# Kernel optimization log

Hardware: AMD Instinct MI355X
Metric: run time of the kernel (lower is better)

Reference implementation:

```python
import jax, jax.numpy as jnp
import numpy as np

H = 64  # hidden size
T, B, I = 512, 4096, 2


def gru_layer(x_seq, Wih, Whh, bih, bhh):
    """PyTorch-semantics GRU layer. x_seq: [T,B,in]. Returns (all_h [T,B,H], h_last [B,H])."""
    # Precompute input-side gates for all timesteps in one GEMM: [T,B,3H]
    xg = jnp.einsum('tbi,gi->tbg', x_seq, Wih) + bih
    h0 = jnp.zeros((x_seq.shape[1], H), dtype=x_seq.dtype)

    def step(h, xg_t):
        hg = h @ Whh.T + bhh  # [B,3H]
        r = jax.nn.sigmoid(xg_t[:, :H] + hg[:, :H])
        z = jax.nn.sigmoid(xg_t[:, H:2 * H] + hg[:, H:2 * H])
        n = jnp.tanh(xg_t[:, 2 * H:] + r * hg[:, 2 * H:])
        h_new = (1.0 - z) * n + z * h
        return h_new, h_new

    h_last, hs = jax.lax.scan(step, h0, xg)
    return hs, h_last


def setup_inputs() -> dict:
    key = jax.random.key(0)
    ks = jax.random.split(key, 12)
    s = 0.125  # ~1/sqrt(H), matches PyTorch uniform init scale
    inp = {
        'x': jax.random.normal(ks[0], (T, B, I), dtype=jnp.float32),
        'Wih0': jax.random.normal(ks[1], (3 * H, I), dtype=jnp.float32) * s,
        'Whh0': jax.random.normal(ks[2], (3 * H, H), dtype=jnp.float32) * s,
        'bih0': jax.random.normal(ks[3], (3 * H,), dtype=jnp.float32) * s,
        'bhh0': jax.random.normal(ks[4], (3 * H,), dtype=jnp.float32) * s,
        'Wih1': jax.random.normal(ks[5], (3 * H, H), dtype=jnp.float32) * s,
        'Whh1': jax.random.normal(ks[6], (3 * H, H), dtype=jnp.float32) * s,
        'bih1': jax.random.normal(ks[7], (3 * H,), dtype=jnp.float32) * s,
        'bhh1': jax.random.normal(ks[8], (3 * H,), dtype=jnp.float32) * s,
        'Wp': jax.random.normal(ks[9], (1, 2 * H), dtype=jnp.float32) * s,
        'bp': jax.random.normal(ks[10], (1,), dtype=jnp.float32) * s,
    }
    return inp


def reference(x, Wih0, Whh0, bih0, bhh0, Wih1, Whh1, bih1, bhh1, Wp, bp):
    hs0, h0f = gru_layer(x, Wih0, Whh0, bih0, bhh0)     # layer 0 over input
    _, h1f = gru_layer(hs0, Wih1, Whh1, bih1, bhh1)      # layer 1 over layer-0 outputs
    feat = jnp.concatenate([h0f, h1f], axis=-1)          # h_n.permute(1,0,2).flatten(1) -> [B, 2H]
    out = feat @ Wp.T + bp                               # [B,1]
    return out.reshape(-1)
```

## Files before the change

### kernel.cpp

```cpp
#include <hip/hip_runtime.h>
#include <stdint.h>

#define TSTEPS 512
#define BATCH  4096

typedef __attribute__((ext_vector_type(8))) short bf16x8;
typedef __attribute__((ext_vector_type(4))) float f32x4;
typedef __attribute__((ext_vector_type(2))) float f32x2;

#define SRZ (-1.4426950408889634f)
#define SN  ( 2.8853900817779268f)
#define SROW 76

__device__ __forceinline__ short f2bf(float f) {
    uint32_t u = __float_as_uint(f);
    uint32_t r = (u + 0x7fffu + ((u >> 16) & 1u)) >> 16;
    return (short)r;
}
__device__ __forceinline__ uint32_t cvt_pk_bf16(float a, float b) {
    uint32_t r;
    asm("v_cvt_pk_bf16_f32 %0, %1, %2" : "=v"(r) : "v"(a), "v"(b));
    return r;
}
__device__ __forceinline__ float fast_rcp(float x) { return __builtin_amdgcn_rcpf(x); }
#if __has_builtin(__builtin_amdgcn_exp2f)
__device__ __forceinline__ float exp2_fast(float x) { return __builtin_amdgcn_exp2f(x); }
#else
__device__ __forceinline__ float exp2_fast(float x) { return __expf(x * 0.6931471805599453f); }
#endif

__device__ __forceinline__ f32x2 fma2(f32x2 a, f32x2 b, f32x2 c) {
    return __builtin_elementwise_fma(a, b, c);
}
__device__ __forceinline__ f32x2 splat2(float s) { return (f32x2){s, s}; }
__device__ __forceinline__ f32x2 exp22(f32x2 y) {
    return (f32x2){exp2_fast(y[0]), exp2_fast(y[1])};
}
__device__ __forceinline__ f32x2 rcp2(f32x2 y) {
    return (f32x2){fast_rcp(y[0]), fast_rcp(y[1])};
}
__device__ __forceinline__ f32x2 sig2(f32x2 y) {
    return rcp2(exp22(y) + splat2(1.0f));
}
__device__ __forceinline__ f32x2 gru_h(f32x2 yz, f32x2 yn, f32x2 h) {
    const f32x2 A = exp22(yz);
    const f32x2 B = exp22(yn);
    const f32x2 P = A * B;
    const f32x2 u = (P - A) + fma2(h, B, h);
    const f32x2 d = (P + A) + (B + splat2(1.0f));
    return u * rcp2(d);
}
__device__ __forceinline__ void bar_lgkm() {
    asm volatile("s_waitcnt lgkmcnt(0)\n\ts_barrier" ::: "memory");
}

__global__ __launch_bounds__(512, 2) void gru_fused(
    const float* __restrict__ x,
    const float* __restrict__ Wih0,
    const float* __restrict__ Whh0,
    const float* __restrict__ bih0,
    const float* __restrict__ bhh0,
    const float* __restrict__ Wih1,
    const float* __restrict__ Whh1,
    const float* __restrict__ bih1,
    const float* __restrict__ bhh1,
    const float* __restrict__ Wp,
    const float* __restrict__ bp,
    float* __restrict__ out)
{
    const int tid  = threadIdx.x;
    const int wv   = tid >> 6;
    const int isL0 = (wv < 4);
    const int w4   = wv & 3;
    const int l    = tid & 63;
    const int lm   = l & 15;
    const int lq   = l >> 4;
    const int b0   = blockIdx.x * 16;
    const int j    = w4 * 16 + lm;

    __shared__ short h0A[2][16 * SROW];
    __shared__ short h1A[2][16 * SROW];
    __shared__ float Pf[16][64];

    for (int idx = tid; idx < 2 * 16 * SROW; idx += 512) {
        ((short*)h0A)[idx] = 0;
        ((short*)h1A)[idx] = 0;
    }
    __syncthreads();

    const int aoff = lm * SROW + lq * 8;
    const int r0   = lq * 4;

    if (isL0) {
        bf16x8 w0[3][2];
#pragma unroll
        for (int g = 0; g < 3; ++g) {
            const int row = g * 64 + j;
            const float sc = (g == 2) ? SN : SRZ;
#pragma unroll
            for (int q = 0; q < 2; ++q) {
                const float* p = Whh0 + row * 64 + q * 32 + lq * 8;
                bf16x8 vh;
#pragma unroll
                for (int i = 0; i < 8; ++i) vh[i] = f2bf(p[i] * sc);
                w0[g][q] = vh;
            }
        }
        const f32x2 wr0 = splat2(SRZ * Wih0[j * 2 + 0]), wr1 = splat2(SRZ * Wih0[j * 2 + 1]);
        const f32x2 wz0 = splat2(SRZ * Wih0[(64 + j) * 2 + 0]), wz1 = splat2(SRZ * Wih0[(64 + j) * 2 + 1]);
        const f32x2 wn0 = splat2(SN * Wih0[(128 + j) * 2 + 0]), wn1 = splat2(SN * Wih0[(128 + j) * 2 + 1]);
        const float cb[3] = { SRZ * (bih0[j] + bhh0[j]),
                              SRZ * (bih0[64 + j] + bhh0[64 + j]),
                              SN  * bhh0[128 + j] };
        const f32x2 bn = splat2(SN * bih0[128 + j]);

        f32x2 h01 = {0.f, 0.f}, h23 = {0.f, 0.f};
        const float* xp = x + (size_t)(b0 + r0) * 2;
        f32x4 xa = *(const f32x4*)xp;
        f32x4 xb = *(const f32x4*)(xp + 4);
        f32x4 xan = xa, xbn = xb;

        for (int t = 0; t <= TSTEPS; ++t) {
            const int pr = t & 1, pw = pr ^ 1;
            bf16x8 a00 = *(const bf16x8*)&h0A[pr][aoff];
            bf16x8 a01 = *(const bf16x8*)&h0A[pr][aoff + 32];

            if (t + 1 < TSTEPS) {
                xp += (size_t)BATCH * 2;
                xan = *(const f32x4*)xp;
                xbn = *(const f32x4*)(xp + 4);
            }

            f32x4 hg0[3];
            __builtin_amdgcn_s_setprio(1);
#pragma unroll
            for (int g = 0; g < 3; ++g) {
                const f32x4 ci = {cb[g], cb[g], cb[g], cb[g]};
                f32x4 c;
                c = __builtin_amdgcn_mfma_f32_16x16x32_bf16(a00, w0[g][0], ci, 0, 0, 0);
                hg0[g] = __builtin_amdgcn_mfma_f32_16x16x32_bf16(a01, w0[g][1], c, 0, 0, 0);
            }
            __builtin_amdgcn_s_setprio(0);

            if (t < TSTEPS) {
                {
                    const f32x2 x0v = {xa[0], xa[2]}, x1v = {xa[1], xa[3]};
                    const f32x2 hgr = {hg0[0][0], hg0[0][1]};
                    const f32x2 hgz = {hg0[1][0], hg0[1][1]};
                    const f32x2 hgn = {hg0[2][0], hg0[2][1]};
                    const f32x2 rv = sig2(fma2(wr0, x0v, fma2(wr1, x1v, hgr)));
                    const f32x2 yz = fma2(wz0, x0v, fma2(wz1, x1v, hgz));
                    const f32x2 yn = fma2(rv, hgn, fma2(wn0, x0v, fma2(wn1, x1v, bn)));
                    const f32x2 hv = gru_h(yz, yn, h01);
                    h01 = hv;
                    const uint32_t pk = cvt_pk_bf16(hv[0], hv[1]);
                    h0A[pw][(r0 + 0) * SROW + j] = (short)(pk & 0xffffu);
                    h0A[pw][(r0 + 1) * SROW + j] = (short)(pk >> 16);
                }
                {
                    const f32x2 x0v = {xb[0], xb[2]}, x1v = {xb[1], xb[3]};
                    const f32x2 hgr = {hg0[0][2], hg0[0][3]};
                    const f32x2 hgz = {hg0[1][2], hg0[1][3]};
                    const f32x2 hgn = {hg0[2][2], hg0[2][3]};
                    const f32x2 rv = sig2(fma2(wr0, x0v, fma2(wr1, x1v, hgr)));
                    const f32x2 yz = fma2(wz0, x0v, fma2(wz1, x1v, hgz));
                    const f32x2 yn = fma2(rv, hgn, fma2(wn0, x0v, fma2(wn1, x1v, bn)));
                    const f32x2 hv = gru_h(yz, yn, h23);
                    h23 = hv;
                    const uint32_t pk = cvt_pk_bf16(hv[0], hv[1]);
                    h0A[pw][(r0 + 2) * SROW + j] = (short)(pk & 0xffffu);
                    h0A[pw][(r0 + 3) * SROW + j] = (short)(pk >> 16);
                }
            }
            xa = xan; xb = xbn;
            bar_lgkm();
        }

        const float wp0 = Wp[j];
        Pf[r0 + 0][j] = wp0 * h01[0];
        Pf[r0 + 1][j] = wp0 * h01[1];
        Pf[r0 + 2][j] = wp0 * h23[0];
        Pf[r0 + 3][j] = wp0 * h23[1];
        __syncthreads();
        __syncthreads();
    } else {
        bf16x8 w1[3][2], w2[3][2];
#pragma unroll
        for (int g = 0; g < 3; ++g) {
            const int row = g * 64 + j;
            const float sc = (g == 2) ? SN : SRZ;
#pragma unroll
            for (int q = 0; q < 2; ++q) {
                const float* p1 = Wih1 + row * 64 + q * 32 + lq * 8;
                const float* p2 = Whh1 + row * 64 + q * 32 + lq * 8;
                bf16x8 v1, v2;
#pragma unroll
                for (int i = 0; i < 8; ++i) {
                    v1[i] = f2bf(p1[i] * sc);
                    v2[i] = f2bf(p2[i] * sc);
                }
                w1[g][q] = v1; w2[g][q] = v2;
            }
        }
        const float cb[3] = { SRZ * (bih1[j] + bhh1[j]),
                              SRZ * (bih1[64 + j] + bhh1[64 + j]),
                              SN  * bih1[128 + j] };
        const float ce2 = SN * bhh1[128 + j];

        f32x2 h01 = {0.f, 0.f}, h23 = {0.f, 0.f};

        for (int t = 0; t <= TSTEPS; ++t) {
            const int pr = t & 1, pw = pr ^ 1;
            bf16x8 a10 = *(const bf16x8*)&h1A[pr][aoff];
            bf16x8 a11 = *(const bf16x8*)&h1A[pr][aoff + 32];

            f32x4 xg1[3], hg1[3];
            __builtin_amdgcn_s_setprio(1);
#pragma unroll
            for (int g = 0; g < 3; ++g) {
                const float ev = (g == 2) ? ce2 : 0.0f;
                const f32x4 ei = {ev, ev, ev, ev};
                f32x4 e;
                e = __builtin_amdgcn_mfma_f32_16x16x32_bf16(a10, w2[g][0], ei, 0, 0, 0);
                hg1[g] = __builtin_amdgcn_mfma_f32_16x16x32_bf16(a11, w2[g][1], e, 0, 0, 0);
            }
            __builtin_amdgcn_s_setprio(0);

            bf16x8 a00 = *(const bf16x8*)&h0A[pr][aoff];
            bf16x8 a01 = *(const bf16x8*)&h0A[pr][aoff + 32];

            __builtin_amdgcn_s_setprio(1);
#pragma unroll
            for (int g = 0; g < 3; ++g) {
                const f32x4 ci = {cb[g], cb[g], cb[g], cb[g]};
                f32x4 d;
                d = __builtin_amdgcn_mfma_f32_16x16x32_bf16(a00, w1[g][0], ci, 0, 0, 0);
                xg1[g] = __builtin_amdgcn_mfma_f32_16x16x32_bf16(a01, w1[g][1], d, 0, 0, 0);
            }
            __builtin_amdgcn_s_setprio(0);

            if (t > 0) {
                {
                    const f32x2 xgr = {xg1[0][0], xg1[0][1]}, hgr = {hg1[0][0], hg1[0][1]};
                    const f32x2 xgz = {xg1[1][0], xg1[1][1]}, hgz = {hg1[1][0], hg1[1][1]};
                    const f32x2 xgn = {xg1[2][0], xg1[2][1]}, hgn = {hg1[2][0], hg1[2][1]};
                    const f32x2 rv = sig2(xgr + hgr);
                    const f32x2 yz = xgz + hgz;
                    const f32x2 yn = fma2(rv, hgn, xgn);
                    const f32x2 hv = gru_h(yz, yn, h01);
                    h01 = hv;
                    const uint32_t pk = cvt_pk_bf16(hv[0], hv[1]);
                    h1A[pw][(r0 + 0) * SROW + j] = (short)(pk & 0xffffu);
                    h1A[pw][(r0 + 1) * SROW + j] = (short)(pk >> 16);
                }
                {
                    const f32x2 xgr = {xg1[0][2], xg1[0][3]}, hgr = {hg1[0][2], hg1[0][3]};
                    const f32x2 xgz = {xg1[1][2], xg1[1][3]}, hgz = {hg1[1][2], hg1[1][3]};
                    const f32x2 xgn = {xg1[2][2], xg1[2][3]}, hgn = {hg1[2][2], hg1[2][3]};
                    const f32x2 rv = sig2(xgr + hgr);
                    const f32x2 yz = xgz + hgz;
                    const f32x2 yn = fma2(rv, hgn, xgn);
                    const f32x2 hv = gru_h(yz, yn, h23);
                    h23 = hv;
                    const uint32_t pk = cvt_pk_bf16(hv[0], hv[1]);
                    h1A[pw][(r0 + 2) * SROW + j] = (short)(pk & 0xffffu);
                    h1A[pw][(r0 + 3) * SROW + j] = (short)(pk >> 16);
                }
            }
            bar_lgkm();
        }

        __syncthreads();
        const float wp1 = Wp[64 + j];
        Pf[r0 + 0][j] += wp1 * h01[0];
        Pf[r0 + 1][j] += wp1 * h01[1];
        Pf[r0 + 2][j] += wp1 * h23[0];
        Pf[r0 + 3][j] += wp1 * h23[1];
        __syncthreads();
    }

    if (tid < 16) {
        float s = bp[0];
#pragma unroll 8
        for (int k = 0; k < 64; ++k) s += Pf[tid][k];
        out[b0 + tid] = s;
    }
}

extern "C" void kernel_launch(void* const* d_in, const int* in_sizes, int n_in,
                              void* d_out, int out_size, void* d_ws, size_t ws_size,
                              hipStream_t stream) {
    (void)in_sizes; (void)n_in; (void)out_size; (void)d_ws; (void)ws_size;
    gru_fused<<<dim3(BATCH / 16), dim3(512), 0, stream>>>(
        (const float*)d_in[0], (const float*)d_in[1], (const float*)d_in[2],
        (const float*)d_in[3], (const float*)d_in[4], (const float*)d_in[5],
        (const float*)d_in[6], (const float*)d_in[7], (const float*)d_in[8],
        (const float*)d_in[9], (const float*)d_in[10], (float*)d_out);
}
```

Before: 337.3 us.

## Unroll GRU time loops by two and precompute layer-0 input gates a step ahead

The layer-0 loop is unrolled by two with even/odd register sets, so the input-projection FMAs for step t+1 are computed while step t's MFMA results are pending. This removes that work from the dependent elementwise chain. Layer 1 is also unrolled by two, with all four LDS A-fragment loads hoisted together and a single priority region around its MFMAs. Its extra trailing iteration is peeled to drop the branch and the unneeded final store. Register pressure rises from the doubled x prefetch and precomputed gate state.

```diff
diff --git a/kernel.cpp b/kernel.cpp
--- a/kernel.cpp
+++ b/kernel.cpp
@@ -3,6 +3,7 @@
 
 #define TSTEPS 512
 #define BATCH  4096
+#define SROW 76
 
 typedef __attribute__((ext_vector_type(8))) short bf16x8;
 typedef __attribute__((ext_vector_type(4))) float f32x4;
@@ -10,7 +11,8 @@
 
 #define SRZ (-1.4426950408889634f)
 #define SN  ( 2.8853900817779268f)
-#define SROW 76
+
+struct PX { f32x2 gr0, gz0, gn0, gr1, gz1, gn1; };
 
 __device__ __forceinline__ short f2bf(float f) {
     uint32_t u = __float_as_uint(f);
@@ -115,22 +117,37 @@
         const f32x2 bn = splat2(SN * bih0[128 + j]);
 
         f32x2 h01 = {0.f, 0.f}, h23 = {0.f, 0.f};
-        const float* xp = x + (size_t)(b0 + r0) * 2;
-        f32x4 xa = *(const f32x4*)xp;
-        f32x4 xb = *(const f32x4*)(xp + 4);
-        f32x4 xan = xa, xbn = xb;
-
-        for (int t = 0; t <= TSTEPS; ++t) {
-            const int pr = t & 1, pw = pr ^ 1;
-            bf16x8 a00 = *(const bf16x8*)&h0A[pr][aoff];
-            bf16x8 a01 = *(const bf16x8*)&h0A[pr][aoff + 32];
-
-            if (t + 1 < TSTEPS) {
+
+        const float* xb_ = x + (size_t)(b0 + r0) * 2;
+        f32x4 xEa = *(const f32x4*)xb_;
+        f32x4 xEb = *(const f32x4*)(xb_ + 4);
+        f32x4 xOa = *(const f32x4*)(xb_ + (size_t)BATCH * 2);
+        f32x4 xOb = *(const f32x4*)(xb_ + (size_t)BATCH * 2 + 4);
+        const float* xp = xb_ + 2 * (size_t)BATCH * 2;
+
+        PX pE, pO;
+        {
+            const f32x2 x0a = {xEa[0], xEa[2]}, x1a = {xEa[1], xEa[3]};
+            const f32x2 x0b = {xEb[0], xEb[2]}, x1b = {xEb[1], xEb[3]};
+            pE.gr0 = fma2(wr0, x0a, wr1 * x1a);
+            pE.gz0 = fma2(wz0, x0a, wz1 * x1a);
+            pE.gn0 = fma2(wn0, x0a, fma2(wn1, x1a, bn));
+            pE.gr1 = fma2(wr0, x0b, wr1 * x1b);
+            pE.gz1 = fma2(wz0, x0b, wz1 * x1b);
+            pE.gn1 = fma2(wn0, x0b, fma2(wn1, x1b, bn));
+        }
+
+        auto l0_step = [&](int pr, bool doload, PX& u, PX& d,
+                           f32x4& xla, f32x4& xlb,
+                           const f32x4& xsa, const f32x4& xsb) {
+            const int pw = pr ^ 1;
+            const bf16x8 a00 = *(const bf16x8*)&h0A[pr][aoff];
+            const bf16x8 a01 = *(const bf16x8*)&h0A[pr][aoff + 32];
+            if (doload) {
+                xla = *(const f32x4*)xp;
+                xlb = *(const f32x4*)(xp + 4);
                 xp += (size_t)BATCH * 2;
-                xan = *(const f32x4*)xp;
-                xbn = *(const f32x4*)(xp + 4);
-            }
-
+            }
             f32x4 hg0[3];
             __builtin_amdgcn_s_setprio(1);
 #pragma unroll
@@ -141,38 +158,45 @@
                 hg0[g] = __builtin_amdgcn_mfma_f32_16x16x32_bf16(a01, w0[g][1], c, 0, 0, 0);
             }
             __builtin_amdgcn_s_setprio(0);
-
-            if (t < TSTEPS) {
-                {
-                    const f32x2 x0v = {xa[0], xa[2]}, x1v = {xa[1], xa[3]};
-                    const f32x2 hgr = {hg0[0][0], hg0[0][1]};
-                    const f32x2 hgz = {hg0[1][0], hg0[1][1]};
-                    const f32x2 hgn = {hg0[2][0], hg0[2][1]};
-                    const f32x2 rv = sig2(fma2(wr0, x0v, fma2(wr1, x1v, hgr)));
-                    const f32x2 yz = fma2(wz0, x0v, fma2(wz1, x1v, hgz));
-                    const f32x2 yn = fma2(rv, hgn, fma2(wn0, x0v, fma2(wn1, x1v, bn)));
-                    const f32x2 hv = gru_h(yz, yn, h01);
-                    h01 = hv;
-                    const uint32_t pk = cvt_pk_bf16(hv[0], hv[1]);
-                    h0A[pw][(r0 + 0) * SROW + j] = (short)(pk & 0xffffu);
-                    h0A[pw][(r0 + 1) * SROW + j] = (short)(pk >> 16);
-                }
-                {
-                    const f32x2 x0v = {xb[0], xb[2]}, x1v = {xb[1], xb[3]};
-                    const f32x2 hgr = {hg0[0][2], hg0[0][3]};
-                    const f32x2 hgz = {hg0[1][2], hg0[1][3]};
-                    const f32x2 hgn = {hg0[2][2], hg0[2][3]};
-                    const f32x2 rv = sig2(fma2(wr0, x0v, fma2(wr1, x1v, hgr)));
-                    const f32x2 yz = fma2(wz0, x0v, fma2(wz1, x1v, hgz));
-                    const f32x2 yn = fma2(rv, hgn, fma2(wn0, x0v, fma2(wn1, x1v, bn)));
-                    const f32x2 hv = gru_h(yz, yn, h23);
-                    h23 = hv;
-                    const uint32_t pk = cvt_pk_bf16(hv[0], hv[1]);
-                    h0A[pw][(r0 + 2) * SROW + j] = (short)(pk & 0xffffu);
-                    h0A[pw][(r0 + 3) * SROW + j] = (short)(pk >> 16);
-                }
-            }
-            xa = xan; xb = xbn;
+            {
+                const f32x2 x0a = {xsa[0], xsa[2]}, x1a = {xsa[1], xsa[3]};
+                const f32x2 x0b = {xsb[0], xsb[2]}, x1b = {xsb[1], xsb[3]};
+                d.gr0 = fma2(wr0, x0a, wr1 * x1a);
+                d.gz0 = fma2(wz0, x0a, wz1 * x1a);
+                d.gn0 = fma2(wn0, x0a, fma2(wn1, x1a, bn));
+                d.gr1 = fma2(wr0, x0b, wr1 * x1b);
+                d.gz1 = fma2(wz0, x0b, wz1 * x1b);
+                d.gn1 = fma2(wn0, x0b, fma2(wn1, x1b, bn));
+            }
+            {
+                const f32x2 hgr = {hg0[0][0], hg0[0][1]};
+                const f32x2 hgz = {hg0[1][0], hg0[1][1]};
+                const f32x2 hgn = {hg0[2][0], hg0[2][1]};
+                const f32x2 rv = sig2(hgr + u.gr0);
+                const f32x2 hv = gru_h(hgz + u.gz0, fma2(rv, hgn, u.gn0), h01);
+                h01 = hv;
+                const uint32_t pk = cvt_pk_bf16(hv[0], hv[1]);
+                h0A[pw][(r0 + 0) * SROW + j] = (short)(pk & 0xffffu);
+                h0A[pw][(r0 + 1) * SROW + j] = (short)(pk >> 16);
+            }
+            {
+                const f32x2 hgr = {hg0[0][2], hg0[0][3]};
+                const f32x2 hgz = {hg0[1][2], hg0[1][3]};
+                const f32x2 hgn = {hg0[2][2], hg0[2][3]};
+                const f32x2 rv = sig2(hgr + u.gr1);
+                const f32x2 hv = gru_h(hgz + u.gz1, fma2(rv, hgn, u.gn1), h23);
+                h23 = hv;
+                const uint32_t pk = cvt_pk_bf16(hv[0], hv[1]);
+                h0A[pw][(r0 + 2) * SROW + j] = (short)(pk & 0xffffu);
+                h0A[pw][(r0 + 3) * SROW + j] = (short)(pk >> 16);
+            }
+        };
+
+        for (int tp = 0; tp < TSTEPS / 2; ++tp) {
+            const bool doload = (tp < TSTEPS / 2 - 1);
+            l0_step(0, doload, pE, pO, xEa, xEb, xOa, xOb);
+            bar_lgkm();
+            l0_step(1, doload, pO, pE, xOa, xOb, xEa, xEb);
             bar_lgkm();
         }
 
@@ -209,10 +233,12 @@
 
         f32x2 h01 = {0.f, 0.f}, h23 = {0.f, 0.f};
 
-        for (int t = 0; t <= TSTEPS; ++t) {
-            const int pr = t & 1, pw = pr ^ 1;
-            bf16x8 a10 = *(const bf16x8*)&h1A[pr][aoff];
-            bf16x8 a11 = *(const bf16x8*)&h1A[pr][aoff + 32];
+        auto l1_step = [&](int pr, bool doew, bool dowrite) {
+            const int pw = pr ^ 1;
+            const bf16x8 a10 = *(const bf16x8*)&h1A[pr][aoff];
+            const bf16x8 a11 = *(const bf16x8*)&h1A[pr][aoff + 32];
+            const bf16x8 a00 = *(const bf16x8*)&h0A[pr][aoff];
+            const bf16x8 a01 = *(const bf16x8*)&h0A[pr][aoff + 32];
 
             f32x4 xg1[3], hg1[3];
             __builtin_amdgcn_s_setprio(1);
@@ -224,12 +250,6 @@
                 e = __builtin_amdgcn_mfma_f32_16x16x32_bf16(a10, w2[g][0], ei, 0, 0, 0);
                 hg1[g] = __builtin_amdgcn_mfma_f32_16x16x32_bf16(a11, w2[g][1], e, 0, 0, 0);
             }
-            __builtin_amdgcn_s_setprio(0);
-
-            bf16x8 a00 = *(const bf16x8*)&h0A[pr][aoff];
-            bf16x8 a01 = *(const bf16x8*)&h0A[pr][aoff + 32];
-
-            __builtin_amdgcn_s_setprio(1);
 #pragma unroll
             for (int g = 0; g < 3; ++g) {
                 const f32x4 ci = {cb[g], cb[g], cb[g], cb[g]};
@@ -239,36 +259,43 @@
             }
             __builtin_amdgcn_s_setprio(0);
 
-            if (t > 0) {
+            if (doew) {
                 {
                     const f32x2 xgr = {xg1[0][0], xg1[0][1]}, hgr = {hg1[0][0], hg1[0][1]};
                     const f32x2 xgz = {xg1[1][0], xg1[1][1]}, hgz = {hg1[1][0], hg1[1][1]};
                     const f32x2 xgn = {xg1[2][0], xg1[2][1]}, hgn = {hg1[2][0], hg1[2][1]};
                     const f32x2 rv = sig2(xgr + hgr);
-                    const f32x2 yz = xgz + hgz;
-                    const f32x2 yn = fma2(rv, hgn, xgn);
-                    const f32x2 hv = gru_h(yz, yn, h01);
+                    const f32x2 hv = gru_h(xgz + hgz, fma2(rv, hgn, xgn), h01);
                     h01 = hv;
-                    const uint32_t pk = cvt_pk_bf16(hv[0], hv[1]);
-                    h1A[pw][(r0 + 0) * SROW + j] = (short)(pk & 0xffffu);
-                    h1A[pw][(r0 + 1) * SROW + j] = (short)(pk >> 16);
+                    if (dowrite) {
+                        const uint32_t pk = cvt_pk_bf16(hv[0], hv[1]);
+                        h1A[pw][(r0 + 0) * SROW + j] = (short)(pk & 0xffffu);
+                        h1A[pw][(r0 + 1) * SROW + j] = (short)(pk >> 16);
+                    }
                 }
                 {
                     const f32x2 xgr = {xg1[0][2], xg1[0][3]}, hgr = {hg1[0][2], hg1[0][3]};
                     const f32x2 xgz = {xg1[1][2], xg1[1][3]}, hgz = {hg1[1][2], hg1[1][3]};
                     const f32x2 xgn = {xg1[2][2], xg1[2][3]}, hgn = {hg1[2][2], hg1[2][3]};
                     const f32x2 rv = sig2(xgr + hgr);
-                    const f32x2 yz = xgz + hgz;
-                    const f32x2 yn = fma2(rv, hgn, xgn);
-                    const f32x2 hv = gru_h(yz, yn, h23);
+                    const f32x2 hv = gru_h(xgz + hgz, fma2(rv, hgn, xgn), h23);
                     h23 = hv;
-                    const uint32_t pk = cvt_pk_bf16(hv[0], hv[1]);
-                    h1A[pw][(r0 + 2) * SROW + j] = (short)(pk & 0xffffu);
-                    h1A[pw][(r0 + 3) * SROW + j] = (short)(pk >> 16);
+                    if (dowrite) {
+                        const uint32_t pk = cvt_pk_bf16(hv[0], hv[1]);
+                        h1A[pw][(r0 + 2) * SROW + j] = (short)(pk & 0xffffu);
+                        h1A[pw][(r0 + 3) * SROW + j] = (short)(pk >> 16);
+                    }
                 }
             }
+        };
+
+        for (int tp = 0; tp < TSTEPS / 2; ++tp) {
+            l1_step(0, tp > 0, true);
             bar_lgkm();
-        }
+            l1_step(1, true, true);
+            bar_lgkm();
+        }
+        l1_step(0, true, false);
 
         __syncthreads();
         const float wp1 = Wp[64 + j];
```

Result: faster. 329.2 us, median of 2 (-2.4%).
